# Performance work log

Measured on AMD Instinct MI355X. Metric: run time of the kernel, lower is better.

The kernel has to match this reference:

```python
import jax, jax.numpy as jnp
import numpy as np

N_NODES = 50000


def _deg_norm(idx, n):
    # DGL GraphConv norm='both': deg.clamp(min=1) ** -0.5
    deg = jax.ops.segment_sum(jnp.ones(idx.shape, jnp.float32), idx, num_segments=n)
    return jnp.clip(deg, 1.0, None) ** -0.5


def _gconv(x, src, dst, W, b, n):
    # h_i = (sum_{j->i} x_j / sqrt(dout_j * din_i)) @ W + b
    h = x * _deg_norm(src, n)[:, None]
    m = jax.ops.segment_sum(h[src], dst, num_segments=n)  # [N, F] SpMM
    m = m * _deg_norm(dst, n)[:, None]
    return m @ W + b


def _gcn3(x, src, dst, W1, b1, W2, b2, W3, b3, n):
    x = jax.nn.relu(_gconv(x, src, dst, W1, b1, n))
    x = jax.nn.relu(_gconv(x, src, dst, W2, b2, n))
    x = jax.nn.relu(_gconv(x, src, dst, W3, b3, n))
    return x


def setup_inputs() -> dict:
    key = jax.random.key(0)
    ks = jax.random.split(key, 16)
    N, E, F_IN, H = N_NODES, 800000, 128, 304
    inp = {}
    for i in range(4):
        inp[f"x{i+1}"] = jax.random.normal(ks[i], (N, F_IN), dtype=jnp.float32)
        inp[f"src{i+1}"] = jax.random.randint(ks[4 + 2 * i], (E,), 0, N, dtype=jnp.int32)
        inp[f"dst{i+1}"] = jax.random.randint(ks[5 + 2 * i], (E,), 0, N, dtype=jnp.int32)
    inp["W1"] = jax.random.normal(ks[12], (F_IN, H), dtype=jnp.float32) / np.sqrt(F_IN)
    inp["b1"] = jnp.zeros((H,), jnp.float32)
    inp["W2"] = jax.random.normal(ks[13], (H, H), dtype=jnp.float32) / np.sqrt(H)
    inp["b2"] = jnp.zeros((H,), jnp.float32)
    inp["W3"] = jax.random.normal(ks[14], (H, H), dtype=jnp.float32) / np.sqrt(H)
    inp["b3"] = jnp.zeros((H,), jnp.float32)
    return inp


def reference(x1, x2, x3, x4, src1, dst1, src2, dst2, src3, dst3, src4, dst4,
              W1, b1, W2, b2, W3, b3):
    n = N_NODES
    h1 = _gcn3(x1, src1, dst1, W1, b1, W2, b2, W3, b3, n)
    h2 = _gcn3(x2, src2, dst2, W1, b1, W2, b2, W3, b3, n)
    h3 = _gcn3(x3, src3, dst3, W1, b1, W2, b2, W3, b3, n)
    h4 = _gcn3(x4, src4, dst4, W1, b1, W2, b2, W3, b3, n)
    # multi_graph_opt='mean': mean over concatenated node axis -> [H]
    x = jnp.mean(jnp.concatenate([h1, h2, h3, h4], axis=0), axis=0)
    # output_opt='mean': scalar
    return jnp.mean(x)
```

## Files before the change

### kernel.cpp

```cpp
#include <hip/hip_runtime.h>
#include <hip/hip_bf16.h>


#define NN 50000
#define EN 800000
#define PEN 950000
#define NCH 64
#define CHE 12500
#define PBS 50016
#define SCB 49
#define DCH 13
#define DCN 4096
#define CPG 391

typedef unsigned int uint;
typedef unsigned short ushort;
typedef unsigned char uchar;
typedef short s8v __attribute__((ext_vector_type(8)));
typedef float f4v __attribute__((ext_vector_type(4)));
typedef float f2v __attribute__((ext_vector_type(2)));
typedef uint u4v __attribute__((ext_vector_type(4)));

__device__ inline ushort f2bf(float f) {
    uint u = __float_as_uint(f);
    uint r = (u + 0x7FFFu + ((u >> 16) & 1u)) >> 16;
    return (ushort)r;
}
__device__ inline uint pk2(float lo, float hi) {
    return (uint)f2bf(lo) | ((uint)f2bf(hi) << 16);
}
__device__ inline f4v mfma16(s8v a, s8v b, f4v c) {
    return __builtin_amdgcn_mfma_f32_16x16x32_bf16(a, b, c, 0, 0, 0);
}
__device__ inline uchar f2fp8(float f) {
    return (uchar)(__builtin_amdgcn_cvt_pk_fp8_f32(f, 0.f, 0, false) & 0xFF);
}
__device__ inline void acc16(u4v d, f2v* a) {
    a[0] += __builtin_amdgcn_cvt_pk_f32_fp8(d.x, false);
    a[1] += __builtin_amdgcn_cvt_pk_f32_fp8(d.x, true);
    a[2] += __builtin_amdgcn_cvt_pk_f32_fp8(d.y, false);
    a[3] += __builtin_amdgcn_cvt_pk_f32_fp8(d.y, true);
    a[4] += __builtin_amdgcn_cvt_pk_f32_fp8(d.z, false);
    a[5] += __builtin_amdgcn_cvt_pk_f32_fp8(d.z, true);
    a[6] += __builtin_amdgcn_cvt_pk_f32_fp8(d.w, false);
    a[7] += __builtin_amdgcn_cvt_pk_f32_fp8(d.w, true);
}

struct GP { const int* p[4]; };
struct FP { const float* p[4]; };


__global__ __launch_bounds__(256) void hist_kernel(GP src, GP dst,
                                                   uint* __restrict__ partS,
                                                   uint* __restrict__ partD) {
    int b = blockIdx.x, dir = blockIdx.y, g = blockIdx.z;
    const int* idx = dir ? dst.p[g] : src.p[g];
    __shared__ uint lh[PBS / 4];
    for (int i = threadIdx.x; i < PBS / 4; i += 256) lh[i] = 0;
    __syncthreads();
    int e0 = b * CHE;
    for (int e = e0 + threadIdx.x; e < e0 + CHE; e += 256) {
        uint n = (uint)idx[e];
        atomicAdd(&lh[n >> 2], 1u << (8 * (n & 3)));
    }
    __syncthreads();
    uint* out = (dir ? partD : partS) + (size_t)(g * NCH + b) * (PBS / 4);
    for (int i = threadIdx.x; i < PBS / 4; i += 256) out[i] = lh[i];
}

__global__ __launch_bounds__(256) void reduce_kernel(const uchar* __restrict__ partS,
                                                     uchar* __restrict__ partD,
                                                     float* __restrict__ ns,
                                                     float* __restrict__ nd,
                                                     int* __restrict__ degd) {
    int idx = blockIdx.x * 256 + threadIdx.x;
    if (idx >= 4 * NN) return;
    int g = idx / NN, n = idx - g * NN;
    const uchar* ps = partS + (size_t)(g * NCH) * PBS + n;
    uint ss = 0;
    for (int b = 0; b < NCH; b++) ss += ps[(size_t)b * PBS];
    uchar* pd = partD + (size_t)(g * NCH) * PBS + n;
    uint run = 0;
    for (int b = 0; b < NCH; b++) {
        uint v = pd[(size_t)b * PBS];
        pd[(size_t)b * PBS] = (uchar)run;
        run += v;
    }
    ns[idx] = rsqrtf((float)max(ss, 1u));
    nd[idx] = rsqrtf((float)max(run, 1u));
    degd[idx] = (int)run;
}

__global__ __launch_bounds__(1024) void scan1_kernel(const int* __restrict__ degd,
                                                     int* __restrict__ rs_all,
                                                     int* __restrict__ bsum) {
    int j = blockIdx.x, g = blockIdx.y;
    int i = j * 1024 + threadIdx.x;
    int v = (i < NN) ? ((degd[g * NN + i] + 3) & ~3) : 0;
    int lane = threadIdx.x & 63, w = threadIdx.x >> 6;
    int x = v;
    #pragma unroll
    for (int off = 1; off < 64; off <<= 1) {
        int t = __shfl_up(x, off, 64);
        if (lane >= off) x += t;
    }
    __shared__ int ws[17];
    if (lane == 63) ws[w] = x;
    __syncthreads();
    if (threadIdx.x == 0) {
        int run = 0;
        #pragma unroll
        for (int k = 0; k < 16; k++) { int t = ws[k]; ws[k] = run; run += t; }
        ws[16] = run;
    }
    __syncthreads();
    if (i < NN) rs_all[g * (NN + 1) + i] = ws[w] + x - v;
    if (threadIdx.x == 0) bsum[g * SCB + j] = ws[16];
}

__global__ void scan2_kernel(int* __restrict__ bsum, int* __restrict__ rs_all) {
    int g = threadIdx.x >> 6, lane = threadIdx.x & 63;
    int v = (lane < SCB) ? bsum[g * SCB + lane] : 0;
    int x = v;
    #pragma unroll
    for (int off = 1; off < 64; off <<= 1) {
        int t = __shfl_up(x, off, 64);
        if (lane >= off) x += t;
    }
    if (lane < SCB) bsum[g * SCB + lane] = x - v;
    if (lane == 63) rs_all[g * (NN + 1) + NN] = x;
}

__global__ __launch_bounds__(1024) void scan3_kernel(const int* __restrict__ bsum,
                                                     int* __restrict__ rs_all) {
    int j = blockIdx.x, g = blockIdx.y;
    int i = j * 1024 + threadIdx.x;
    int off = bsum[g * SCB + j];
    if (i < NN) rs_all[g * (NN + 1) + i] += off;
}

__global__ __launch_bounds__(256) void cfill_kernel(uint* __restrict__ csr2) {
    int i = blockIdx.x * 256 + threadIdx.x;
    if (i < 4 * PEN / 2) csr2[i] = (uint)NN | ((uint)NN << 16);
}

__global__ __launch_bounds__(256) void scatter_kernel(GP src, GP dst,
                                                      const int* __restrict__ rs_all,
                                                      const uchar* __restrict__ pf,
                                                      ushort* __restrict__ csr) {
    int b = blockIdx.x, g = blockIdx.y;
    __shared__ uint lc[PBS / 4];
    for (int i = threadIdx.x; i < PBS / 4; i += 256) lc[i] = 0;
    __syncthreads();
    const int* sp = src.p[g];
    const int* dp = dst.p[g];
    const int* rs = rs_all + g * (NN + 1);
    const uchar* pfb = pf + (size_t)(g * NCH + b) * PBS;
    ushort* csrg = csr + (size_t)g * PEN;
    int e0 = b * CHE;
    for (int e = e0 + threadIdx.x; e < e0 + CHE; e += 256) {
        uint d = (uint)dp[e];
        int s = sp[e];
        uint sh = 8 * (d & 3);
        uint old = atomicAdd(&lc[d >> 2], 1u << sh);
        uint r = (old >> sh) & 0xFFu;
        csrg[rs[d] + (int)pfb[d] + (int)r] = (ushort)s;
    }
}


__global__ __launch_bounds__(256) void dhist_kernel(const int* __restrict__ degd,
                                                    int* __restrict__ dhp) {
    int b = blockIdx.x, g = blockIdx.y;
    __shared__ int lh[256];
    lh[threadIdx.x] = 0;
    __syncthreads();
    int n0 = b * DCN, nend = min(n0 + DCN, NN);
    for (int i = n0 + threadIdx.x; i < nend; i += 256) {
        int d = degd[g * NN + i];
        atomicAdd(&lh[d < 255 ? d : 255], 1);
    }
    __syncthreads();
    dhp[(g * DCH + b) * 256 + threadIdx.x] = lh[threadIdx.x];
}

__global__ void dscan_kernel(int* __restrict__ dhp, int* __restrict__ dbase) {
    int tid = threadIdx.x, lane = tid & 63, w = tid >> 6;
    __shared__ int ws[4];
    for (int g = 0; g < 4; g++) {
        int run = 0;
        for (int c = 0; c < DCH; c++) {
            int v = dhp[(g * DCH + c) * 256 + tid];
            dhp[(g * DCH + c) * 256 + tid] = run;
            run += v;
        }
        int x = run;
        #pragma unroll
        for (int off = 1; off < 64; off <<= 1) {
            int t = __shfl_up(x, off, 64);
            if (lane >= off) x += t;
        }
        if (lane == 63) ws[w] = x;
        __syncthreads();
        int prefix = 0;
        for (int j = 0; j < w; j++) prefix += ws[j];
        dbase[g * 256 + tid] = prefix + x - run;
        __syncthreads();
    }
}

__global__ __launch_bounds__(256) void dscatter_kernel(const int* __restrict__ degd,
                                                       const int* __restrict__ dhp,
                                                       const int* __restrict__ dbase,
                                                       int* __restrict__ perm) {
    int b = blockIdx.x, g = blockIdx.y;
    __shared__ int lc[256];
    lc[threadIdx.x] = 0;
    __syncthreads();
    int n0 = b * DCN, nend = min(n0 + DCN, NN);
    for (int i = n0 + threadIdx.x; i < nend; i += 256) {
        int d = degd[g * NN + i];
        d = d < 255 ? d : 255;
        int r = atomicAdd(&lc[d], 1);
        int pos = dbase[g * 256 + d] + dhp[(g * DCH + b) * 256 + d] + r;
        perm[g * NN + pos] = i;
    }
}


__global__ void padzero_kernel(uint* __restrict__ xs, int nxs,
                               uint* __restrict__ hb, int nhb) {
    int t = threadIdx.x;
    if (t < nxs * 16) xs[(size_t)(t >> 4) * (NN + 1) * 16 + (size_t)NN * 16 + (t & 15)] = 0;
    if (t < nhb * 16) hb[(size_t)(t >> 4) * (NN + 1) * 16 + (size_t)NN * 16 + (t & 15)] = 0;
}


__global__ __launch_bounds__(256) void wtrans_kernel(const float* __restrict__ W,
                                                     ushort* __restrict__ Wt,
                                                     int Kreal, int WS) {
    int idx = blockIdx.x * 256 + threadIdx.x;
    if (idx >= 320 * WS) return;
    int n = idx / WS, k = idx - n * WS;
    float v = (n < 304 && k < Kreal) ? W[k * 304 + n] : 0.f;
    Wt[idx] = f2bf(v);
}


__global__ __launch_bounds__(256) void prescale_kernel(FP xp,
                                                       const float* __restrict__ ns,
                                                       uint* __restrict__ xs) {
    int g = blockIdx.y;
    const float* x = xp.p[g];
    ns += (size_t)g * NN;
    xs += (size_t)g * 2 * (NN + 1) * 16;
    int idx = blockIdx.x * 256 + threadIdx.x;
    if (idx >= NN * 16) return;
    int row = idx >> 4, j = idx & 15;
    int sl = j >> 3, pos = j & 7;
    float nv = ns[row];
    float4 v0 = ((const float4*)x)[idx * 2];
    float4 v1 = ((const float4*)x)[idx * 2 + 1];
    int p0 = 0, p1 = 0;
    p0 = __builtin_amdgcn_cvt_pk_fp8_f32(v0.x * nv, v0.y * nv, p0, false);
    p0 = __builtin_amdgcn_cvt_pk_fp8_f32(v0.z * nv, v0.w * nv, p0, true);
    p1 = __builtin_amdgcn_cvt_pk_fp8_f32(v1.x * nv, v1.y * nv, p1, false);
    p1 = __builtin_amdgcn_cvt_pk_fp8_f32(v1.z * nv, v1.w * nv, p1, true);
    ((uint2*)xs)[(size_t)sl * (NN + 1) * 8 + row * 8 + pos] = make_uint2((uint)p0, (uint)p1);
}

__global__ __launch_bounds__(256) void spmm_kernel(const u4v* __restrict__ xsl,
                                                   const int* __restrict__ prs,
                                                   const ushort* __restrict__ csr,
                                                   const float* __restrict__ nd,
                                                   const int* __restrict__ perm,
                                                   u4v* __restrict__ out,
                                                   int ostride) {
    int g = blockIdx.z, SL = gridDim.y;
    xsl += (size_t)g * SL * (NN + 1) * 4;
    prs += (size_t)g * (NN + 1);
    csr += (size_t)g * PEN;
    nd  += (size_t)g * NN;
    perm += (size_t)g * NN;
    out += (size_t)g * NN * ostride;

    int wv = threadIdx.x >> 6, lane = threadIdx.x & 63;
    int grp = lane >> 2, gl = lane & 3;
    int slot = blockIdx.x * 64 + wv * 16 + grp;
    int sl = blockIdx.y;
    const u4v* base = xsl + (size_t)sl * (NN + 1) * 4 + gl;
    bool ok = slot < NN;
    int node = ok ? perm[slot] : 0;
    int p0 = ok ? prs[node] : 0, p1 = ok ? prs[node + 1] : 0;
    f2v a[8], b[8];
    #pragma unroll
    for (int i = 0; i < 8; i++) { a[i] = (f2v){0.f, 0.f}; b[i] = (f2v){0.f, 0.f}; }
    int e = p0;
    if ((p1 - p0) & 4) {
        uint2 e4 = *(const uint2*)(csr + e);
        uint s0 = e4.x & 0xFFFFu, s1 = e4.x >> 16;
        uint s2 = e4.y & 0xFFFFu, s3 = e4.y >> 16;
        u4v d0 = base[s0 * 4];
        u4v d1 = base[s1 * 4];
        u4v d2 = base[s2 * 4];
        u4v d3 = base[s3 * 4];
        acc16(d0, a); acc16(d1, b); acc16(d2, a); acc16(d3, b);
        e += 4;
    }
    for (; e < p1; e += 8) {
        uint2 q0 = *(const uint2*)(csr + e);
        uint2 q1 = *(const uint2*)(csr + e + 4);
        uint s0 = q0.x & 0xFFFFu, s1 = q0.x >> 16;
        uint s2 = q0.y & 0xFFFFu, s3 = q0.y >> 16;
        uint s4 = q1.x & 0xFFFFu, s5 = q1.x >> 16;
        uint s6 = q1.y & 0xFFFFu, s7 = q1.y >> 16;
        u4v d0 = base[s0 * 4];
        u4v d1 = base[s1 * 4];
        u4v d2 = base[s2 * 4];
        u4v d3 = base[s3 * 4];
        u4v d4 = base[s4 * 4];
        u4v d5 = base[s5 * 4];
        u4v d6 = base[s6 * 4];
        u4v d7 = base[s7 * 4];
        acc16(d0, a); acc16(d1, b); acc16(d2, a); acc16(d3, b);
        acc16(d4, a); acc16(d5, b); acc16(d6, a); acc16(d7, b);
    }
    if (ok) {
        float nv = nd[node];
        f2v nv2 = {nv, nv};
        f2v c0 = (a[0] + b[0]) * nv2, c1 = (a[1] + b[1]) * nv2;
        f2v c2 = (a[2] + b[2]) * nv2, c3 = (a[3] + b[3]) * nv2;
        f2v c4 = (a[4] + b[4]) * nv2, c5 = (a[5] + b[5]) * nv2;
        f2v c6 = (a[6] + b[6]) * nv2, c7 = (a[7] + b[7]) * nv2;
        u4v o0, o1;
        o0.x = pk2(c0[0], c0[1]); o0.y = pk2(c1[0], c1[1]);
        o0.z = pk2(c2[0], c2[1]); o0.w = pk2(c3[0], c3[1]);
        o1.x = pk2(c4[0], c4[1]); o1.y = pk2(c5[0], c5[1]);
        o1.z = pk2(c6[0], c6[1]); o1.w = pk2(c7[0], c7[1]);
        u4v* op = out + (size_t)node * ostride + sl * 8 + gl * 2;
        __builtin_nontemporal_store(o0, op);
        __builtin_nontemporal_store(o1, op + 1);
    }
}


template<int KSTEPS, bool REDUCE>
__global__ __launch_bounds__(256) void gemm_kernel(const ushort* __restrict__ A, int astride,
                                                   const ushort* __restrict__ Wt,
                                                   const float* __restrict__ bias,
                                                   const float* __restrict__ ns,
                                                   uchar* __restrict__ Hout,
                                                   double* __restrict__ accum,
                                                   int CH) {
    constexpr int K = KSTEPS * 32;
    constexpr int WS = K + 8;
    int b = blockIdx.x;
    int r8 = b & 7;
    int nt4 = (b >> 3) & 3;
    int grp = b >> 5;
    int chunk = grp * 8 + r8;
    if (chunk >= CH) return;
    int g = chunk / CPG, rc = chunk - g * CPG;
    int M = NN;

    __shared__ __align__(16) ushort wt[80 * WS];
    __shared__ float redbuf[4];
    A += (size_t)g * NN * astride;
    int tid = threadIdx.x, lane = tid & 63, wv = tid >> 6;
    int nb = nt4 * 80;
    int r0 = rc * 128 + wv * 32;

    {
        const s8v* src = (const s8v*)(Wt + (size_t)nb * WS);
        s8v* dst = (s8v*)wt;
        for (int i = tid; i < 80 * WS / 8; i += 256) dst[i] = src[i];
    }
    __syncthreads();

    f4v acc[2][5];
    #pragma unroll
    for (int t = 0; t < 2; t++)
        #pragma unroll
        for (int j = 0; j < 5; j++) acc[t][j] = (f4v){0.f, 0.f, 0.f, 0.f};

    int m15 = lane & 15;
    int kq = (lane >> 4) * 8;
    int ar0 = min(r0 + m15, M - 1);
    int ar1 = min(r0 + 16 + m15, M - 1);
    const ushort* a0p = A + (size_t)ar0 * astride + kq;
    const ushort* a1p = A + (size_t)ar1 * astride + kq;
    const ushort* bb = wt + (size_t)m15 * WS + kq;

    #pragma unroll
    for (int ks = 0; ks < KSTEPS; ks++) {
        s8v af0 = *(const s8v*)(a0p + ks * 32);
        s8v af1 = *(const s8v*)(a1p + ks * 32);
        #pragma unroll
        for (int nt = 0; nt < 5; nt++) {
            s8v bf = *(const s8v*)(bb + nt * 16 * WS + ks * 32);
            acc[0][nt] = mfma16(af0, bf, acc[0][nt]);
            acc[1][nt] = mfma16(af1, bf, acc[1][nt]);
        }
    }

    int rq = (lane >> 4) * 4;
    if constexpr (!REDUCE) {
        const float* nsg = ns + (size_t)g * NN;
        uchar* hg = Hout + (size_t)g * 5 * (NN + 1) * 64;
        float nsv[2][4];
        #pragma unroll
        for (int t = 0; t < 2; t++)
            #pragma unroll
            for (int r = 0; r < 4; r++) {
                int row = r0 + t * 16 + rq + r;
                nsv[t][r] = (row < M) ? nsg[row] : 0.f;
            }
        #pragma unroll
        for (int nt = 0; nt < 5; nt++) {
            int col = nb + nt * 16 + m15;
            float bv = (col < 304) ? bias[col] : 0.f;
            int sl = col >> 6, cw = col & 63;
            uchar* hp = hg + (size_t)sl * (NN + 1) * 64 + cw;
            #pragma unroll
            for (int t = 0; t < 2; t++)
                #pragma unroll
                for (int r = 0; r < 4; r++) {
                    int row = r0 + t * 16 + rq + r;
                    if (row < M) {
                        float y = fmaxf(acc[t][nt][r] + bv, 0.f) * nsv[t][r];
                        hp[(size_t)row * 64] = f2fp8(y);
                    }
                }
        }
    } else {
        float s = 0.f;
        #pragma unroll
        for (int nt = 0; nt < 5; nt++) {
            int col = nb + nt * 16 + m15;
            float bv = (col < 304) ? bias[col] : 0.f;
            #pragma unroll
            for (int t = 0; t < 2; t++)
                #pragma unroll
                for (int r = 0; r < 4; r++) {
                    int row = r0 + t * 16 + rq + r;
                    if (row < M && col < 304) s += fmaxf(acc[t][nt][r] + bv, 0.f);
                }
        }
        #pragma unroll
        for (int off = 32; off; off >>= 1) s += __shfl_xor(s, off, 64);
        if (lane == 0) redbuf[wv] = s;
        __syncthreads();
        if (tid == 0) {
            double bsum = (double)redbuf[0] + redbuf[1] + redbuf[2] + redbuf[3];
            atomicAdd(accum, bsum);
        }
    }
}

__global__ void finalize_kernel(const double* __restrict__ accum, float* __restrict__ out) {
    out[0] = (float)(accum[0] / (double)(4.0 * NN * 304.0));
}


extern "C" void kernel_launch(void* const* d_in, const int* in_sizes, int n_in,
                              void* d_out, int out_size, void* d_ws, size_t ws_size,
                              hipStream_t stream) {
    char* w = (char*)d_ws;
    auto alloc = [&](size_t bytes) {
        char* p = w;
        w += (bytes + 255) & ~(size_t)255;
        return p;
    };
    double* accum  = (double*)alloc(256);
    int*    degd   = (int*)alloc((size_t)4 * NN * 4);
    int*    rs     = (int*)alloc((size_t)4 * (NN + 1) * 4);
    int*    bsum   = (int*)alloc((size_t)4 * SCB * 4);
    float*  nsrc   = (float*)alloc((size_t)4 * NN * 4);
    float*  ndst   = (float*)alloc((size_t)4 * NN * 4);
    ushort* csr    = (ushort*)alloc((size_t)4 * PEN * 2);
    int*    dhp    = (int*)alloc((size_t)4 * DCH * 256 * 4);
    int*    dbase  = (int*)alloc((size_t)4 * 256 * 4);
    int*    perm   = (int*)alloc((size_t)4 * NN * 4);
    ushort* wt1    = (ushort*)alloc((size_t)320 * 136 * 2);
    ushort* wt2    = (ushort*)alloc((size_t)320 * 328 * 2);
    ushort* wt3    = (ushort*)alloc((size_t)320 * 328 * 2);
    uint*   partS  = (uint*)alloc((size_t)4 * NCH * PBS);
    uint*   partD  = (uint*)alloc((size_t)4 * NCH * PBS);

    size_t need_tail = ((size_t)4 * 5 * (NN + 1) * 64 + 255 + (size_t)4 * NN * 320 * 2 + 255);
    size_t used = (size_t)(w - (char*)d_ws);
    bool batched = (ws_size >= used + need_tail + 4096);

    uint *hbuf, *mbuf, *xs, *m1;
    if (batched) {
        hbuf = (uint*)alloc((size_t)4 * 5 * (NN + 1) * 64);
        mbuf = (uint*)alloc((size_t)4 * NN * 320 * 2);
        xs   = partS;
        m1   = mbuf;
    } else {
        hbuf = (uint*)alloc((size_t)5 * (NN + 1) * 64);
        mbuf = (uint*)alloc((size_t)NN * 320 * 2);
        xs   = partS;
        m1   = partD;
    }

    (void)hipMemsetAsync(accum, 0, 256, stream);

    wtrans_kernel<<<(320 * 136 + 255) / 256, 256, 0, stream>>>((const float*)d_in[12], wt1, 128, 136);
    wtrans_kernel<<<(320 * 328 + 255) / 256, 256, 0, stream>>>((const float*)d_in[14], wt2, 304, 328);
    wtrans_kernel<<<(320 * 328 + 255) / 256, 256, 0, stream>>>((const float*)d_in[16], wt3, 304, 328);

    GP S, D;
    FP X;
    for (int g = 0; g < 4; g++) {
        S.p[g] = (const int*)d_in[1 + 3 * g];
        D.p[g] = (const int*)d_in[2 + 3 * g];
        X.p[g] = (const float*)d_in[3 * g];
    }
    hist_kernel<<<dim3(NCH, 2, 4), 256, 0, stream>>>(S, D, partS, partD);
    reduce_kernel<<<(4 * NN + 255) / 256, 256, 0, stream>>>((const uchar*)partS, (uchar*)partD,
                                                            nsrc, ndst, degd);
    scan1_kernel<<<dim3(SCB, 4), 1024, 0, stream>>>(degd, rs, bsum);
    scan2_kernel<<<1, 256, 0, stream>>>(bsum, rs);
    scan3_kernel<<<dim3(SCB, 4), 1024, 0, stream>>>(bsum, rs);
    cfill_kernel<<<(4 * PEN / 2 + 255) / 256, 256, 0, stream>>>((uint*)csr);
    scatter_kernel<<<dim3(NCH, 4), 256, 0, stream>>>(S, D, rs, (const uchar*)partD, csr);
    dhist_kernel<<<dim3(DCH, 4), 256, 0, stream>>>(degd, dhp);
    dscan_kernel<<<1, 256, 0, stream>>>(dhp, dbase);
    dscatter_kernel<<<dim3(DCH, 4), 256, 0, stream>>>(degd, dhp, dbase, perm);
    padzero_kernel<<<1, 512, 0, stream>>>(xs, batched ? 8 : 2, hbuf, batched ? 20 : 5);

    const float* b1 = (const float*)d_in[13];
    const float* b2 = (const float*)d_in[15];
    const float* b3 = (const float*)d_in[17];

    if (batched) {
        dim3 pgrid((NN * 16 + 255) / 256, 4);
        dim3 sgrid1((NN + 63) / 64, 2, 4);
        dim3 sgrid2((NN + 63) / 64, 5, 4);
        int CH = 4 * CPG;
        int BG = ((CH + 7) / 8) * 32;
        prescale_kernel<<<pgrid, 256, 0, stream>>>(X, nsrc, xs);
        spmm_kernel<<<sgrid1, 256, 0, stream>>>((const u4v*)xs, rs, csr,
                                                ndst, perm, (u4v*)m1, 16);
        gemm_kernel<4, false><<<BG, 256, 0, stream>>>((const ushort*)m1, 128, wt1, b1, nsrc,
                                                      (uchar*)hbuf, nullptr, CH);
        spmm_kernel<<<sgrid2, 256, 0, stream>>>((const u4v*)hbuf, rs, csr,
                                                ndst, perm, (u4v*)mbuf, 40);
        gemm_kernel<10, false><<<BG, 256, 0, stream>>>((const ushort*)mbuf, 320, wt2, b2, nsrc,
                                                       (uchar*)hbuf, nullptr, CH);
        spmm_kernel<<<sgrid2, 256, 0, stream>>>((const u4v*)hbuf, rs, csr,
                                                ndst, perm, (u4v*)mbuf, 40);
        gemm_kernel<10, true><<<BG, 256, 0, stream>>>((const ushort*)mbuf, 320, wt3, b3, nullptr,
                                                      nullptr, accum, CH);
    } else {
        dim3 pgrid((NN * 16 + 255) / 256, 1);
        dim3 sgrid1((NN + 63) / 64, 2);
        dim3 sgrid2((NN + 63) / 64, 5);
        int CH = CPG;
        int BG = ((CH + 7) / 8) * 32;
        for (int g = 0; g < 4; g++) {
            FP Xg;
            Xg.p[0] = Xg.p[1] = Xg.p[2] = Xg.p[3] = (const float*)d_in[3 * g];
            const float* nsg = nsrc + g * NN;
            const float* ndg = ndst + g * NN;
            const int* rsg = rs + g * (NN + 1);
            const ushort* csrg = csr + (size_t)g * PEN;
            const int* permg = perm + g * NN;

            prescale_kernel<<<pgrid, 256, 0, stream>>>(Xg, nsg, xs);
            spmm_kernel<<<sgrid1, 256, 0, stream>>>((const u4v*)xs, rsg, csrg,
                                                    ndg, permg, (u4v*)m1, 16);
            gemm_kernel<4, false><<<BG, 256, 0, stream>>>((const ushort*)m1, 128, wt1, b1, nsg,
                                                          (uchar*)hbuf, nullptr, CH);
            spmm_kernel<<<sgrid2, 256, 0, stream>>>((const u4v*)hbuf, rsg, csrg,
                                                    ndg, permg, (u4v*)mbuf, 40);
            gemm_kernel<10, false><<<BG, 256, 0, stream>>>((const ushort*)mbuf, 320, wt2, b2, nsg,
                                                           (uchar*)hbuf, nullptr, CH);
            spmm_kernel<<<sgrid2, 256, 0, stream>>>((const u4v*)hbuf, rsg, csrg,
                                                    ndg, permg, (u4v*)mbuf, 40);
            gemm_kernel<10, true><<<BG, 256, 0, stream>>>((const ushort*)mbuf, 320, wt3, b3, nullptr,
                                                          nullptr, accum, CH);
        }
    }
    finalize_kernel<<<1, 1, 0, stream>>>(accum, (float*)d_out);
}
```

Baseline: 1.033 ms.

## Pin SpMM (graph, slice) pairs to XCDs and stream CSR with nontemporal loads

In the batched path, the SpMM launch becomes a flat 1D grid. Block indices are remapped so that each (graph, feature-slice) pair, or half of one, lands on a fixed XCD (block index mod 8). This keeps each pair's gathered feature slice resident in one XCD's L2 rather than duplicated across all eight. CSR index reads become nontemporal loads so they do not evict the gathered features. The risk is load imbalance across XCDs from the fixed assignment and interleaved node halves, and it relies on round-robin block dispatch to XCDs.

```diff
diff --git a/kernel.cpp b/kernel.cpp
--- a/kernel.cpp
+++ b/kernel.cpp
@@ -20,6 +20,7 @@
 typedef float f4v __attribute__((ext_vector_type(4)));
 typedef float f2v __attribute__((ext_vector_type(2)));
 typedef uint u4v __attribute__((ext_vector_type(4)));
+typedef uint u2v __attribute__((ext_vector_type(2)));
 
 __device__ inline ushort f2bf(float f) {
     uint u = __float_as_uint(f);
@@ -269,14 +270,32 @@
     ((uint2*)xs)[(size_t)sl * (NN + 1) * 8 + row * 8 + pos] = make_uint2((uint)p0, (uint)p1);
 }
 
+template<bool PINNED>
 __global__ __launch_bounds__(256) void spmm_kernel(const u4v* __restrict__ xsl,
                                                    const int* __restrict__ prs,
                                                    const ushort* __restrict__ csr,
                                                    const float* __restrict__ nd,
                                                    const int* __restrict__ perm,
                                                    u4v* __restrict__ out,
-                                                   int ostride) {
-    int g = blockIdx.z, SL = gridDim.y;
+                                                   int ostride, int SL, int UH,
+                                                   int NSG, int HLV) {
+    int wv = threadIdx.x >> 6, lane = threadIdx.x & 63;
+    int grp = lane >> 2, gl = lane & 3;
+    int g, sl, slot;
+    if constexpr (PINNED) {
+        int b = blockIdx.x;
+        int r = b & 7, k = b >> 3;
+        int hpl = k / UH, unit = k - hpl * UH;
+        int hp = hpl * 8 + r;
+        int pair = hp % NSG;
+        int h = hp / NSG;
+        g = pair / SL; sl = pair - g * SL;
+        int base = unit * 64 + wv * 16 + grp;
+        slot = HLV ? base * 2 + h : base;
+    } else {
+        g = blockIdx.z; sl = blockIdx.y; SL = gridDim.y;
+        slot = blockIdx.x * 64 + wv * 16 + grp;
+    }
     xsl += (size_t)g * SL * (NN + 1) * 4;
     prs += (size_t)g * (NN + 1);
     csr += (size_t)g * PEN;
@@ -284,32 +303,28 @@
     perm += (size_t)g * NN;
     out += (size_t)g * NN * ostride;
 
-    int wv = threadIdx.x >> 6, lane = threadIdx.x & 63;
-    int grp = lane >> 2, gl = lane & 3;
-    int slot = blockIdx.x * 64 + wv * 16 + grp;
-    int sl = blockIdx.y;
     const u4v* base = xsl + (size_t)sl * (NN + 1) * 4 + gl;
     bool ok = slot < NN;
     int node = ok ? perm[slot] : 0;
     int p0 = ok ? prs[node] : 0, p1 = ok ? prs[node + 1] : 0;
-    f2v a[8], b[8];
+    f2v a[8], b2[8];
     #pragma unroll
-    for (int i = 0; i < 8; i++) { a[i] = (f2v){0.f, 0.f}; b[i] = (f2v){0.f, 0.f}; }
+    for (int i = 0; i < 8; i++) { a[i] = (f2v){0.f, 0.f}; b2[i] = (f2v){0.f, 0.f}; }
     int e = p0;
     if ((p1 - p0) & 4) {
-        uint2 e4 = *(const uint2*)(csr + e);
+        u2v e4 = __builtin_nontemporal_load((const u2v*)(csr + e));
         uint s0 = e4.x & 0xFFFFu, s1 = e4.x >> 16;
         uint s2 = e4.y & 0xFFFFu, s3 = e4.y >> 16;
         u4v d0 = base[s0 * 4];
         u4v d1 = base[s1 * 4];
         u4v d2 = base[s2 * 4];
         u4v d3 = base[s3 * 4];
-        acc16(d0, a); acc16(d1, b); acc16(d2, a); acc16(d3, b);
+        acc16(d0, a); acc16(d1, b2); acc16(d2, a); acc16(d3, b2);
         e += 4;
     }
     for (; e < p1; e += 8) {
-        uint2 q0 = *(const uint2*)(csr + e);
-        uint2 q1 = *(const uint2*)(csr + e + 4);
+        u2v q0 = __builtin_nontemporal_load((const u2v*)(csr + e));
+        u2v q1 = __builtin_nontemporal_load((const u2v*)(csr + e + 4));
         uint s0 = q0.x & 0xFFFFu, s1 = q0.x >> 16;
         uint s2 = q0.y & 0xFFFFu, s3 = q0.y >> 16;
         uint s4 = q1.x & 0xFFFFu, s5 = q1.x >> 16;
@@ -322,16 +337,16 @@
         u4v d5 = base[s5 * 4];
         u4v d6 = base[s6 * 4];
         u4v d7 = base[s7 * 4];
-        acc16(d0, a); acc16(d1, b); acc16(d2, a); acc16(d3, b);
-        acc16(d4, a); acc16(d5, b); acc16(d6, a); acc16(d7, b);
+        acc16(d0, a); acc16(d1, b2); acc16(d2, a); acc16(d3, b2);
+        acc16(d4, a); acc16(d5, b2); acc16(d6, a); acc16(d7, b2);
     }
     if (ok) {
         float nv = nd[node];
         f2v nv2 = {nv, nv};
-        f2v c0 = (a[0] + b[0]) * nv2, c1 = (a[1] + b[1]) * nv2;
-        f2v c2 = (a[2] + b[2]) * nv2, c3 = (a[3] + b[3]) * nv2;
-        f2v c4 = (a[4] + b[4]) * nv2, c5 = (a[5] + b[5]) * nv2;
-        f2v c6 = (a[6] + b[6]) * nv2, c7 = (a[7] + b[7]) * nv2;
+        f2v c0 = (a[0] + b2[0]) * nv2, c1 = (a[1] + b2[1]) * nv2;
+        f2v c2 = (a[2] + b2[2]) * nv2, c3 = (a[3] + b2[3]) * nv2;
+        f2v c4 = (a[4] + b2[4]) * nv2, c5 = (a[5] + b2[5]) * nv2;
+        f2v c6 = (a[6] + b2[6]) * nv2, c7 = (a[7] + b2[7]) * nv2;
         u4v o0, o1;
         o0.x = pk2(c0[0], c0[1]); o0.y = pk2(c1[0], c1[1]);
         o0.z = pk2(c2[0], c2[1]); o0.w = pk2(c3[0], c3[1]);
@@ -536,21 +551,21 @@
 
     if (batched) {
         dim3 pgrid((NN * 16 + 255) / 256, 4);
-        dim3 sgrid1((NN + 63) / 64, 2, 4);
-        dim3 sgrid2((NN + 63) / 64, 5, 4);
+        int B1 = 8 * 1 * 782;
+        int B2 = 8 * 5 * 391;
         int CH = 4 * CPG;
         int BG = ((CH + 7) / 8) * 32;
         prescale_kernel<<<pgrid, 256, 0, stream>>>(X, nsrc, xs);
-        spmm_kernel<<<sgrid1, 256, 0, stream>>>((const u4v*)xs, rs, csr,
-                                                ndst, perm, (u4v*)m1, 16);
+        spmm_kernel<true><<<B1, 256, 0, stream>>>((const u4v*)xs, rs, csr, ndst, perm,
+                                                  (u4v*)m1, 16, 2, 782, 8, 0);
         gemm_kernel<4, false><<<BG, 256, 0, stream>>>((const ushort*)m1, 128, wt1, b1, nsrc,
                                                       (uchar*)hbuf, nullptr, CH);
-        spmm_kernel<<<sgrid2, 256, 0, stream>>>((const u4v*)hbuf, rs, csr,
-                                                ndst, perm, (u4v*)mbuf, 40);
+        spmm_kernel<true><<<B2, 256, 0, stream>>>((const u4v*)hbuf, rs, csr, ndst, perm,
+                                                  (u4v*)mbuf, 40, 5, 391, 20, 1);
         gemm_kernel<10, false><<<BG, 256, 0, stream>>>((const ushort*)mbuf, 320, wt2, b2, nsrc,
                                                        (uchar*)hbuf, nullptr, CH);
-        spmm_kernel<<<sgrid2, 256, 0, stream>>>((const u4v*)hbuf, rs, csr,
-                                                ndst, perm, (u4v*)mbuf, 40);
+        spmm_kernel<true><<<B2, 256, 0, stream>>>((const u4v*)hbuf, rs, csr, ndst, perm,
+                                                  (u4v*)mbuf, 40, 5, 391, 20, 1);
         gemm_kernel<10, true><<<BG, 256, 0, stream>>>((const ushort*)mbuf, 320, wt3, b3, nullptr,
                                                       nullptr, accum, CH);
     } else {
@@ -569,16 +584,16 @@
             const int* permg = perm + g * NN;
 
             prescale_kernel<<<pgrid, 256, 0, stream>>>(Xg, nsg, xs);
-            spmm_kernel<<<sgrid1, 256, 0, stream>>>((const u4v*)xs, rsg, csrg,
-                                                    ndg, permg, (u4v*)m1, 16);
+            spmm_kernel<false><<<sgrid1, 256, 0, stream>>>((const u4v*)xs, rsg, csrg,
+                                                           ndg, permg, (u4v*)m1, 16, 0, 0, 0, 0);
             gemm_kernel<4, false><<<BG, 256, 0, stream>>>((const ushort*)m1, 128, wt1, b1, nsg,
                                                           (uchar*)hbuf, nullptr, CH);
-            spmm_kernel<<<sgrid2, 256, 0, stream>>>((const u4v*)hbuf, rsg, csrg,
-                                                    ndg, permg, (u4v*)mbuf, 40);
+            spmm_kernel<false><<<sgrid2, 256, 0, stream>>>((const u4v*)hbuf, rsg, csrg,
+                                                           ndg, permg, (u4v*)mbuf, 40, 0, 0, 0, 0);
             gemm_kernel<10, false><<<BG, 256, 0, stream>>>((const ushort*)mbuf, 320, wt2, b2, nsg,
                                                            (uchar*)hbuf, nullptr, CH);
-            spmm_kernel<<<sgrid2, 256, 0, stream>>>((const u4v*)hbuf, rsg, csrg,
-                                                    ndg, permg, (u4v*)mbuf, 40);
+            spmm_kernel<false><<<sgrid2, 256, 0, stream>>>((const u4v*)hbuf, rsg, csrg,
+                                                           ndg, permg, (u4v*)mbuf, 40, 0, 0, 0, 0);
             gemm_kernel<10, true><<<BG, 256, 0, stream>>>((const ushort*)mbuf, 320, wt3, b3, nullptr,
                                                           nullptr, accum, CH);
         }
```

Result: slower. 1.059 ms (+2.5%).
